# Optimization experiments

Measured on AMD Instinct MI355X. Metric: run time of the kernel, lower is better.

Reference implementation:

```python
import jax, jax.numpy as jnp
import numpy as np


def setup_inputs() -> dict:
    key = jax.random.key(0)
    kx, kw = jax.random.split(key)
    B, IN, OUT = 8192, 4096, 4096
    x = jax.random.normal(kx, (B, IN), dtype=jnp.float32)
    # matches torch init: (rand*2-1)*0.001 -> uniform in [-0.001, 0.001]
    weight = jax.random.uniform(kw, (OUT, IN), dtype=jnp.float32, minval=-1.0, maxval=1.0) * 0.001
    return {"x": x, "weight": weight}


def reference(x, weight):
    # scaling factor = mean(|W|), detached
    scale = jax.lax.stop_gradient(jnp.mean(jnp.abs(weight)))
    binary_no_grad = scale * jnp.sign(weight)
    clipped = jnp.clip(weight, -1.0, 1.0)
    # straight-through estimator: fwd value = scale*sign(W), bwd grad = d(clip)/dW
    binary_weights = jax.lax.stop_gradient(binary_no_grad - clipped) + clipped
    # F.linear: y = x @ W^T  -> [B, OUT]
    return jnp.einsum('bi,oi->bo', x, binary_weights)
```

## Files before the change

kernel.cpp:

```cpp
#include <hip/hip_runtime.h>
#include <hip/hip_bf16.h>
#include <stdint.h>

typedef __attribute__((ext_vector_type(4))) int i32x4;

#define GLOAD(g, l) __builtin_amdgcn_global_load_lds(                      \
    (const __attribute__((address_space(1))) void*)(g),                    \
    (__attribute__((address_space(3))) void*)(l), 16, 0, 0)

#define MFMAI8 __builtin_amdgcn_mfma_i32_16x16x64_i8
#define BARRIER __builtin_amdgcn_s_barrier
#define LGKM0 asm volatile("s_waitcnt lgkmcnt(0)" ::: "memory")
#define LGKM8 asm volatile("s_waitcnt lgkmcnt(8)" ::: "memory")

__global__ __launch_bounds__(256) void wsign_kernel(
    const float* __restrict__ W, char* __restrict__ S,
    float* __restrict__ partials) {
  const int tid = threadIdx.x;
  const int idx = blockIdx.x * 256 + tid;
  const float4* wp = reinterpret_cast<const float4*>(W) + (size_t)idx * 4;
  float s = 0.f;
  int out[4];
#pragma unroll
  for (int i = 0; i < 4; ++i) {
    float4 w = wp[i];
    int b0 = (w.x > 0.f) - (w.x < 0.f);
    int b1 = (w.y > 0.f) - (w.y < 0.f);
    int b2 = (w.z > 0.f) - (w.z < 0.f);
    int b3 = (w.w > 0.f) - (w.w < 0.f);
    out[i] = (b0 & 255) | ((b1 & 255) << 8) | ((b2 & 255) << 16) |
             ((b3 & 255) << 24);
    s += fabsf(w.x) + fabsf(w.y) + fabsf(w.z) + fabsf(w.w);
  }
  reinterpret_cast<int4*>(S)[idx] =
      make_int4(out[0], out[1], out[2], out[3]);
#pragma unroll
  for (int off = 32; off > 0; off >>= 1) s += __shfl_down(s, off, 64);
  __shared__ float sm[4];
  if ((tid & 63) == 0) sm[tid >> 6] = s;
  __syncthreads();
  if (tid == 0) partials[blockIdx.x] = sm[0] + sm[1] + sm[2] + sm[3];
}

__global__ __launch_bounds__(256) void xquant_kernel(
    const float* __restrict__ X, char* __restrict__ XQ,
    float* __restrict__ qrow) {
  const int row = blockIdx.x;
  const int tid = threadIdx.x;
  const float4* xr = reinterpret_cast<const float4*>(X + (size_t)row * 4096);
  float4 v[4];
  float am = 0.f;
#pragma unroll
  for (int i = 0; i < 4; ++i) {
    v[i] = xr[tid * 4 + i];
    am = fmaxf(am, fmaxf(fmaxf(fabsf(v[i].x), fabsf(v[i].y)),
                         fmaxf(fabsf(v[i].z), fabsf(v[i].w))));
  }
#pragma unroll
  for (int off = 1; off < 64; off <<= 1)
    am = fmaxf(am, __shfl_xor(am, off, 64));
  __shared__ float wm[4];
  if ((tid & 63) == 0) wm[tid >> 6] = am;
  __syncthreads();
  float amax = fmaxf(fmaxf(wm[0], wm[1]), fmaxf(wm[2], wm[3]));
  amax = fmaxf(amax, 1e-20f);
  const float rq = 127.f / amax;
  int out[4];
#pragma unroll
  for (int i = 0; i < 4; ++i) {
    int b0 = __float2int_rn(v[i].x * rq);
    int b1 = __float2int_rn(v[i].y * rq);
    int b2 = __float2int_rn(v[i].z * rq);
    int b3 = __float2int_rn(v[i].w * rq);
    out[i] = (b0 & 255) | ((b1 & 255) << 8) | ((b2 & 255) << 16) |
             ((b3 & 255) << 24);
  }
  reinterpret_cast<int4*>(XQ + (size_t)row * 4096)[tid] =
      make_int4(out[0], out[1], out[2], out[3]);
  if (tid == 0) qrow[row] = amax * (1.f / 127.f);
}

__global__ __launch_bounds__(256) void finalize_kernel(
    const float* __restrict__ partials, float* __restrict__ scale) {
  const int tid = threadIdx.x;
  float s = 0.f;
  for (int i = tid; i < 4096; i += 256) s += partials[i];
#pragma unroll
  for (int off = 32; off > 0; off >>= 1) s += __shfl_down(s, off, 64);
  __shared__ float sm[4];
  if ((tid & 63) == 0) sm[tid >> 6] = s;
  __syncthreads();
  if (tid == 0) scale[0] = (sm[0] + sm[1] + sm[2] + sm[3]) * (1.0f / 16777216.0f);
}

__global__ __launch_bounds__(512, 2) void gemm_i8_kernel(
    const char* __restrict__ A,
    const char* __restrict__ B,
    const float* __restrict__ scale_p, const float* __restrict__ qrow,
    float* __restrict__ C) {
  constexpr int M = 8192, N = 4096, K = 4096;
  constexpr int NT = K / 128;
  constexpr int NI = NT / 2;
  __shared__ __align__(16) char lds[131072];

  const int tid = threadIdx.x;
  const int wid = tid >> 6;
  const int lane = tid & 63;
  const int wr = wid >> 2;
  const int wc = wid & 3;
  const int bh = wc >> 1;
  const int bsub = (wc & 1) * 8192;
  const int fr = lane & 15;
  const int fq = lane >> 4;
  const int sk0 = ((fq) ^ (fr & 7)) * 16;
  const int sk1 = ((4 + fq) ^ (fr & 7)) * 16;

  const int bid = blockIdx.x;
  const int swz = (bid & 7) * 64 + (bid >> 3);
  const int tm = swz >> 4, tn = swz & 15;

  const int srow = tid >> 3;
  const int sg = (tid & 7) ^ (srow & 7);
  const char* aSrc0 = A + (size_t)(tm * 256 + srow) * K + sg * 16;
  const char* aSrc1 = aSrc0 + (size_t)128 * K;
  const char* bSrc0 = B + (size_t)(tn * 256 + srow) * K + sg * 16;
  const char* bSrc1 = bSrc0 + (size_t)128 * K;

#define STAGE(srcBase, slotIdx, koff)                              \
  do {                                                             \
    const char* _s = (srcBase) + (koff);                           \
    char* _d = lds + (slotIdx) * 16384 + wid * 1024;               \
    GLOAD(_s, _d);                                                 \
    GLOAD(_s + (size_t)64 * K, _d + 8192);                         \
  } while (0)

  const char* aSp0 = lds + (0 + wr) * 16384 + fr * 128;
  const char* aSp1 = lds + (2 + wr) * 16384 + fr * 128;
  const char* bSp0 = lds + (4 + bh) * 16384 + bsub + fr * 128;
  const char* bSp1 = lds + (6 + bh) * 16384 + bsub + fr * 128;

  i32x4 acc[8][4];
#pragma unroll
  for (int m = 0; m < 8; ++m)
#pragma unroll
    for (int n = 0; n < 4; ++n) acc[m][n] = (i32x4){0, 0, 0, 0};

#define RD_B(bS)                                                       \
  _Pragma("unroll") for (int n = 0; n < 4; ++n) {                      \
    bq[n][0] = *(const i32x4*)((bS) + n * 2048 + sk0);                 \
    bq[n][1] = *(const i32x4*)((bS) + n * 2048 + sk1);                 \
  }
#define RD_A(aS, q)                                                    \
  _Pragma("unroll") for (int m2 = 0; m2 < 2; ++m2) {                   \
    av[m2][0] = *(const i32x4*)((aS) + (2 * (q) + m2) * 2048 + sk0);   \
    av[m2][1] = *(const i32x4*)((aS) + (2 * (q) + m2) * 2048 + sk1);   \
  }
#define QMFMA(q)                                                       \
  do {                                                                 \
    __builtin_amdgcn_s_setprio(1);                                     \
    _Pragma("unroll") for (int m2 = 0; m2 < 2; ++m2)                   \
        _Pragma("unroll") for (int n = 0; n < 4; ++n) {                \
      acc[2 * (q) + m2][n] =                                           \
          MFMAI8(av[m2][0], bq[n][0], acc[2 * (q) + m2][n], 0, 0, 0);  \
      acc[2 * (q) + m2][n] =                                           \
          MFMAI8(av[m2][1], bq[n][1], acc[2 * (q) + m2][n], 0, 0, 0);  \
    }                                                                  \
    __builtin_amdgcn_s_setprio(0);                                     \
  } while (0)

  STAGE(bSrc0, 4, 0);
  STAGE(bSrc1, 5, 0);
  STAGE(aSrc0, 0, 0);
  STAGE(aSrc1, 1, 0);
  STAGE(bSrc0, 6, 128);
  STAGE(bSrc1, 7, 128);
  asm volatile("s_waitcnt vmcnt(4)" ::: "memory");
  BARRIER();

  for (int i = 0; i < NI; ++i) {
    const int t0 = 2 * i;
    const int k1 = (t0 + 1) * 128, k2 = (t0 + 2) * 128, k3 = (t0 + 3) * 128;
    i32x4 bq[4][2], av[2][2];

    RD_B(bSp0);
    RD_A(aSp0, 0);
    STAGE(aSrc0, 2, k1);
    LGKM8;
    BARRIER(); LGKM0; QMFMA(0); BARRIER();

    RD_A(aSp0, 1);
    STAGE(aSrc1, 3, k1);
    BARRIER(); LGKM0; QMFMA(1); BARRIER();

    RD_A(aSp0, 2);
    if (t0 + 2 < NT) STAGE(bSrc0, 4, k2);
    BARRIER(); LGKM0; QMFMA(2); BARRIER();

    RD_A(aSp0, 3);
    if (t0 + 2 < NT) {
      STAGE(bSrc1, 5, k2);
      asm volatile("s_waitcnt vmcnt(4)" ::: "memory");
    } else {
      asm volatile("s_waitcnt vmcnt(0)" ::: "memory");
    }
    BARRIER(); LGKM0; QMFMA(3); BARRIER();

    RD_B(bSp1);
    RD_A(aSp1, 0);
    if (t0 + 2 < NT) STAGE(aSrc0, 0, k2);
    LGKM8;
    BARRIER(); LGKM0; QMFMA(0); BARRIER();

    RD_A(aSp1, 1);
    if (t0 + 2 < NT) STAGE(aSrc1, 1, k2);
    BARRIER(); LGKM0; QMFMA(1); BARRIER();

    RD_A(aSp1, 2);
    if (t0 + 3 < NT) STAGE(bSrc0, 6, k3);
    BARRIER(); LGKM0; QMFMA(2); BARRIER();

    RD_A(aSp1, 3);
    if (t0 + 3 < NT) {
      STAGE(bSrc1, 7, k3);
      asm volatile("s_waitcnt vmcnt(4)" ::: "memory");
    }
    BARRIER(); LGKM0; QMFMA(3); BARRIER();
  }

  const float sc = *scale_p;
  const int crow0 = tm * 256 + wr * 128 + fq * 4;
  const int ccol0 = tn * 256 + wc * 64 + fr;
#pragma unroll
  for (int m = 0; m < 8; ++m) {
    const int row = crow0 + m * 16;
    float q[4];
#pragma unroll
    for (int j = 0; j < 4; ++j) q[j] = sc * qrow[row + j];
#pragma unroll
    for (int n = 0; n < 4; ++n) {
      i32x4 v = acc[m][n];
      float* cp = C + (size_t)row * N + ccol0 + n * 16;
#pragma unroll
      for (int j = 0; j < 4; ++j) cp[(size_t)j * N] = (float)v[j] * q[j];
    }
  }
#undef STAGE
#undef RD_A
#undef RD_B
#undef QMFMA
}

extern "C" void kernel_launch(void* const* d_in, const int* in_sizes, int n_in,
                              void* d_out, int out_size, void* d_ws,
                              size_t ws_size, hipStream_t stream) {
  const float* x = (const float*)d_in[0];
  const float* w = (const float*)d_in[1];
  float* out = (float*)d_out;

  char* ws = (char*)d_ws;
  char* xq = ws;
  char* sq = ws + 33554432;
  float* qrow = (float*)(ws + 50331648);
  float* partials = (float*)(ws + 50331648 + 32768);
  float* scale = (float*)(ws + 50331648 + 32768 + 16384);

  wsign_kernel<<<4096, 256, 0, stream>>>(w, sq, partials);
  xquant_kernel<<<8192, 256, 0, stream>>>(x, xq, qrow);
  finalize_kernel<<<1, 256, 0, stream>>>(partials, scale);
  gemm_i8_kernel<<<512, 512, 0, stream>>>(xq, sq, scale, qrow, out);
}
```

Baseline: 177.8 us.

## Shrink int8 GEMM tile to 128x128 with simple double-buffered K=64 pipeline

Replaces the 256x256 block tile with a 128x128 tile over K steps of 64. It uses a simple two-slot LDS double buffer (32KB) and launches 2048 blocks instead of 512, targeting four blocks per CU for occupancy. This removes the elaborate phased schedule and XOR swizzle, trading it for higher occupancy and simpler code. In exchange, global traffic per FLOP roughly doubles, the unswizzled 64-byte-stride LDS reads may cause bank conflicts, and the barrier count per K step rises relative to compute.

```diff
diff --git a/kernel.cpp b/kernel.cpp
--- a/kernel.cpp
+++ b/kernel.cpp
@@ -11,7 +11,6 @@
 #define MFMAI8 __builtin_amdgcn_mfma_i32_16x16x64_i8
 #define BARRIER __builtin_amdgcn_s_barrier
 #define LGKM0 asm volatile("s_waitcnt lgkmcnt(0)" ::: "memory")
-#define LGKM8 asm volatile("s_waitcnt lgkmcnt(8)" ::: "memory")
 
 __global__ __launch_bounds__(256) void wsign_kernel(
     const float* __restrict__ W, char* __restrict__ S,
@@ -93,161 +92,97 @@
   if (tid == 0) scale[0] = (sm[0] + sm[1] + sm[2] + sm[3]) * (1.0f / 16777216.0f);
 }
 
-__global__ __launch_bounds__(512, 2) void gemm_i8_kernel(
+__global__ __launch_bounds__(512, 4) void gemm_i8_kernel(
     const char* __restrict__ A,
     const char* __restrict__ B,
     const float* __restrict__ scale_p, const float* __restrict__ qrow,
     float* __restrict__ C) {
   constexpr int M = 8192, N = 4096, K = 4096;
-  constexpr int NT = K / 128;
-  constexpr int NI = NT / 2;
-  __shared__ __align__(16) char lds[131072];
+  constexpr int NT = K / 64;
+  __shared__ __align__(16) char lds[32768];
 
   const int tid = threadIdx.x;
   const int wid = tid >> 6;
   const int lane = tid & 63;
   const int wr = wid >> 2;
   const int wc = wid & 3;
-  const int bh = wc >> 1;
-  const int bsub = (wc & 1) * 8192;
   const int fr = lane & 15;
   const int fq = lane >> 4;
-  const int sk0 = ((fq) ^ (fr & 7)) * 16;
-  const int sk1 = ((4 + fq) ^ (fr & 7)) * 16;
 
   const int bid = blockIdx.x;
-  const int swz = (bid & 7) * 64 + (bid >> 3);
-  const int tm = swz >> 4, tn = swz & 15;
-
-  const int srow = tid >> 3;
-  const int sg = (tid & 7) ^ (srow & 7);
-  const char* aSrc0 = A + (size_t)(tm * 256 + srow) * K + sg * 16;
-  const char* aSrc1 = aSrc0 + (size_t)128 * K;
-  const char* bSrc0 = B + (size_t)(tn * 256 + srow) * K + sg * 16;
-  const char* bSrc1 = bSrc0 + (size_t)128 * K;
-
-#define STAGE(srcBase, slotIdx, koff)                              \
-  do {                                                             \
-    const char* _s = (srcBase) + (koff);                           \
-    char* _d = lds + (slotIdx) * 16384 + wid * 1024;               \
-    GLOAD(_s, _d);                                                 \
-    GLOAD(_s + (size_t)64 * K, _d + 8192);                         \
-  } while (0)
-
-  const char* aSp0 = lds + (0 + wr) * 16384 + fr * 128;
-  const char* aSp1 = lds + (2 + wr) * 16384 + fr * 128;
-  const char* bSp0 = lds + (4 + bh) * 16384 + bsub + fr * 128;
-  const char* bSp1 = lds + (6 + bh) * 16384 + bsub + fr * 128;
-
-  i32x4 acc[8][4];
-#pragma unroll
-  for (int m = 0; m < 8; ++m)
-#pragma unroll
-    for (int n = 0; n < 4; ++n) acc[m][n] = (i32x4){0, 0, 0, 0};
-
-#define RD_B(bS)                                                       \
-  _Pragma("unroll") for (int n = 0; n < 4; ++n) {                      \
-    bq[n][0] = *(const i32x4*)((bS) + n * 2048 + sk0);                 \
-    bq[n][1] = *(const i32x4*)((bS) + n * 2048 + sk1);                 \
-  }
-#define RD_A(aS, q)                                                    \
-  _Pragma("unroll") for (int m2 = 0; m2 < 2; ++m2) {                   \
-    av[m2][0] = *(const i32x4*)((aS) + (2 * (q) + m2) * 2048 + sk0);   \
-    av[m2][1] = *(const i32x4*)((aS) + (2 * (q) + m2) * 2048 + sk1);   \
-  }
-#define QMFMA(q)                                                       \
-  do {                                                                 \
-    __builtin_amdgcn_s_setprio(1);                                     \
-    _Pragma("unroll") for (int m2 = 0; m2 < 2; ++m2)                   \
-        _Pragma("unroll") for (int n = 0; n < 4; ++n) {                \
-      acc[2 * (q) + m2][n] =                                           \
-          MFMAI8(av[m2][0], bq[n][0], acc[2 * (q) + m2][n], 0, 0, 0);  \
-      acc[2 * (q) + m2][n] =                                           \
-          MFMAI8(av[m2][1], bq[n][1], acc[2 * (q) + m2][n], 0, 0, 0);  \
-    }                                                                  \
-    __builtin_amdgcn_s_setprio(0);                                     \
-  } while (0)
-
-  STAGE(bSrc0, 4, 0);
-  STAGE(bSrc1, 5, 0);
-  STAGE(aSrc0, 0, 0);
-  STAGE(aSrc1, 1, 0);
-  STAGE(bSrc0, 6, 128);
-  STAGE(bSrc1, 7, 128);
-  asm volatile("s_waitcnt vmcnt(4)" ::: "memory");
-  BARRIER();
-
-  for (int i = 0; i < NI; ++i) {
-    const int t0 = 2 * i;
-    const int k1 = (t0 + 1) * 128, k2 = (t0 + 2) * 128, k3 = (t0 + 3) * 128;
-    i32x4 bq[4][2], av[2][2];
-
-    RD_B(bSp0);
-    RD_A(aSp0, 0);
-    STAGE(aSrc0, 2, k1);
-    LGKM8;
-    BARRIER(); LGKM0; QMFMA(0); BARRIER();
-
-    RD_A(aSp0, 1);
-    STAGE(aSrc1, 3, k1);
-    BARRIER(); LGKM0; QMFMA(1); BARRIER();
-
-    RD_A(aSp0, 2);
-    if (t0 + 2 < NT) STAGE(bSrc0, 4, k2);
-    BARRIER(); LGKM0; QMFMA(2); BARRIER();
-
-    RD_A(aSp0, 3);
-    if (t0 + 2 < NT) {
-      STAGE(bSrc1, 5, k2);
-      asm volatile("s_waitcnt vmcnt(4)" ::: "memory");
+  const int swz = (bid & 7) * 256 + (bid >> 3);
+  const int tm = swz >> 5, tn = swz & 31;
+
+  const char* aSrc = A + (size_t)(tm * 128 + (tid >> 2)) * K + (tid & 3) * 16;
+  const char* bSrc = B + (size_t)(tn * 128 + (tid >> 2)) * K + (tid & 3) * 16;
+  char* aDst = lds + tid * 16;
+  char* bDst = lds + 16384 + tid * 16;
+
+  const char* aBase = lds + (wr * 64 + fr) * 64 + fq * 16;
+  const char* bBase = lds + 16384 + (wc * 32 + fr) * 64 + fq * 16;
+
+  i32x4 acc[4][2];
+#pragma unroll
+  for (int m = 0; m < 4; ++m)
+#pragma unroll
+    for (int n = 0; n < 2; ++n) acc[m][n] = (i32x4){0, 0, 0, 0};
+
+  GLOAD(aSrc, aDst);
+  GLOAD(bSrc, bDst);
+  GLOAD(aSrc + 64, aDst + 8192);
+  GLOAD(bSrc + 64, bDst + 8192);
+
+  for (int t = 0; t < NT; ++t) {
+    const int par = t & 1;
+    const char* aB = aBase + par * 8192;
+    const char* bB = bBase + par * 8192;
+    if (t == NT - 1) {
+      asm volatile("s_waitcnt vmcnt(0)" ::: "memory");
     } else {
-      asm volatile("s_waitcnt vmcnt(0)" ::: "memory");
+      asm volatile("s_waitcnt vmcnt(2)" ::: "memory");
     }
-    BARRIER(); LGKM0; QMFMA(3); BARRIER();
-
-    RD_B(bSp1);
-    RD_A(aSp1, 0);
-    if (t0 + 2 < NT) STAGE(aSrc0, 0, k2);
-    LGKM8;
-    BARRIER(); LGKM0; QMFMA(0); BARRIER();
-
-    RD_A(aSp1, 1);
-    if (t0 + 2 < NT) STAGE(aSrc1, 1, k2);
-    BARRIER(); LGKM0; QMFMA(1); BARRIER();
-
-    RD_A(aSp1, 2);
-    if (t0 + 3 < NT) STAGE(bSrc0, 6, k3);
-    BARRIER(); LGKM0; QMFMA(2); BARRIER();
-
-    RD_A(aSp1, 3);
-    if (t0 + 3 < NT) {
-      STAGE(bSrc1, 7, k3);
-      asm volatile("s_waitcnt vmcnt(4)" ::: "memory");
+    BARRIER();
+
+    i32x4 bq[2], av[4];
+    bq[0] = *(const i32x4*)(bB);
+    bq[1] = *(const i32x4*)(bB + 1024);
+#pragma unroll
+    for (int m = 0; m < 4; ++m) av[m] = *(const i32x4*)(aB + m * 1024);
+
+    __builtin_amdgcn_s_setprio(1);
+#pragma unroll
+    for (int m = 0; m < 4; ++m)
+#pragma unroll
+      for (int n = 0; n < 2; ++n)
+        acc[m][n] = MFMAI8(av[m], bq[n], acc[m][n], 0, 0, 0);
+    __builtin_amdgcn_s_setprio(0);
+
+    LGKM0;
+    BARRIER();
+
+    if (t + 2 < NT) {
+      GLOAD(aSrc + (t + 2) * 64, aDst + par * 8192);
+      GLOAD(bSrc + (t + 2) * 64, bDst + par * 8192);
     }
-    BARRIER(); LGKM0; QMFMA(3); BARRIER();
   }
 
   const float sc = *scale_p;
-  const int crow0 = tm * 256 + wr * 128 + fq * 4;
-  const int ccol0 = tn * 256 + wc * 64 + fr;
-#pragma unroll
-  for (int m = 0; m < 8; ++m) {
+  const int crow0 = tm * 128 + wr * 64 + fq * 4;
+  const int ccol0 = tn * 128 + wc * 32 + fr;
+#pragma unroll
+  for (int m = 0; m < 4; ++m) {
     const int row = crow0 + m * 16;
     float q[4];
 #pragma unroll
     for (int j = 0; j < 4; ++j) q[j] = sc * qrow[row + j];
 #pragma unroll
-    for (int n = 0; n < 4; ++n) {
+    for (int n = 0; n < 2; ++n) {
       i32x4 v = acc[m][n];
       float* cp = C + (size_t)row * N + ccol0 + n * 16;
 #pragma unroll
       for (int j = 0; j < 4; ++j) cp[(size_t)j * N] = (float)v[j] * q[j];
     }
   }
-#undef STAGE
-#undef RD_A
-#undef RD_B
-#undef QMFMA
 }
 
 extern "C" void kernel_launch(void* const* d_in, const int* in_sizes, int n_in,
@@ -267,5 +202,5 @@
   wsign_kernel<<<4096, 256, 0, stream>>>(w, sq, partials);
   xquant_kernel<<<8192, 256, 0, stream>>>(x, xq, qrow);
   finalize_kernel<<<1, 256, 0, stream>>>(partials, scale);
-  gemm_i8_kernel<<<512, 512, 0, stream>>>(xq, sq, scale, qrow, out);
-}
+  gemm_i8_kernel<<<2048, 512, 0, stream>>>(xq, sq, scale, qrow, out);
+}
```

Result: slower. 239.2 us (+34.5%).
